# Performance work log

Hardware: AMD Instinct MI355X
Metric: run time of the kernel (lower is better)

## Reference

```python
import jax, jax.numpy as jnp
import numpy as np

B, N, E, D, H = 8, 50000, 200000, 64, 8

def setup_inputs() -> dict:
    key = jax.random.key(0)
    ks = jax.random.split(key, 6)
    X = jax.random.normal(ks[0], (B, N, D), dtype=jnp.float32)
    Ri_idx = jax.random.randint(ks[1], (B, E), 0, N, dtype=jnp.int64)
    Ro_idx = jax.random.randint(ks[2], (B, E), 0, N, dtype=jnp.int64)
    # MLP params: Linear(2D -> H), tanh, Linear(H -> 1), sigmoid
    W1 = jax.random.normal(ks[3], (2 * D, H), dtype=jnp.float32) * (1.0 / np.sqrt(2 * D))
    b1 = jnp.zeros((H,), dtype=jnp.float32)
    W2 = jax.random.normal(ks[4], (H, 1), dtype=jnp.float32) * (1.0 / np.sqrt(H))
    b2 = jnp.zeros((1,), dtype=jnp.float32)
    return {"X": X, "Ri_idx": Ri_idx, "Ro_idx": Ro_idx, "W1": W1, "b1": b1, "W2": W2, "b2": b2}

def reference(X, Ri_idx, Ro_idx, W1, b1, W2, b2):
    # spmm with one-hot incidence rows == gather of node features per edge
    bi = jnp.take_along_axis(X, Ri_idx[:, :, None], axis=1)  # [B,E,D]
    bo = jnp.take_along_axis(X, Ro_idx[:, :, None], axis=1)  # [B,E,D]
    Bfeat = jnp.concatenate([bo, bi], axis=-1)               # [B,E,2D]
    h = jnp.tanh(jnp.einsum('bed,dh->beh', Bfeat, W1) + b1)  # [B,E,H]
    out = jax.nn.sigmoid(jnp.einsum('beh,ho->beo', h, W2) + b2)  # [B,E,1]
    return out.squeeze(-1)  # [B,E]
```

## Files before the change

### kernel.cpp

```cpp
#include <hip/hip_runtime.h>
#include <hip/hip_bf16.h>

#define TILE 256

__device__ __forceinline__ float fast_tanh(float x) {
    float ax = fabsf(x);
    float t = __expf(-2.f * ax);
    float r = (1.f - t) * __builtin_amdgcn_rcpf(1.f + t);
    return copysignf(r, x);
}

__device__ __forceinline__ float fast_sigmoid(float s) {
    return __builtin_amdgcn_rcpf(1.f + __expf(-s));
}

__global__ __launch_bounds__(256, 2) void phase1_kernel(
    const float* __restrict__ X, const float* __restrict__ W1,
    const float* __restrict__ b1, float* __restrict__ P, int BN) {
    __shared__ float4 tile[TILE * 16];
    int t = threadIdx.x;
    int base = blockIdx.x * TILE;

#pragma unroll
    for (int k = 0; k < 16; ++k) {
        int s = t + (k << 8);
        int node = s >> 4;
        int f4 = s & 15;
        int gnode = base + node;
        gnode = (gnode < BN) ? gnode : (BN - 1);
        float4 v = *(const float4*)(X + ((size_t)gnode << 6) + (f4 << 2));
        tile[(node << 4) | (f4 ^ (node & 15))] = v;
    }
    __syncthreads();

    float acc[16];
#pragma unroll
    for (int j = 0; j < 8; ++j) acc[j] = b1[j];
#pragma unroll
    for (int j = 8; j < 16; ++j) acc[j] = 0.f;

    const float4* row = tile + (t << 4);
    int sw = t & 15;
#pragma unroll
    for (int dc4 = 0; dc4 < 16; ++dc4) {
        float4 xv = row[dc4 ^ sw];
#pragma unroll
        for (int dd = 0; dd < 4; ++dd) {
            int d = (dc4 << 2) + dd;
            float xs = (dd == 0) ? xv.x : (dd == 1) ? xv.y : (dd == 2) ? xv.z : xv.w;
            const float* wo = W1 + d * 8;
            const float* wi = W1 + (64 + d) * 8;
#pragma unroll
            for (int j = 0; j < 8; ++j) {
                acc[j]     += xs * wo[j];
                acc[8 + j] += xs * wi[j];
            }
        }
    }

    int gnode = base + t;
    if (gnode < BN) {
        float4* dst = (float4*)(P + ((size_t)gnode << 4));
        dst[0] = make_float4(acc[0],  acc[1],  acc[2],  acc[3]);
        dst[1] = make_float4(acc[4],  acc[5],  acc[6],  acc[7]);
        dst[2] = make_float4(acc[8],  acc[9],  acc[10], acc[11]);
        dst[3] = make_float4(acc[12], acc[13], acc[14], acc[15]);
    }
}

__global__ __launch_bounds__(256) void phase2_kernel(
    const int* __restrict__ Ri, const int* __restrict__ Ro,
    const float* __restrict__ P, const float* __restrict__ W2,
    const float* __restrict__ b2, float* __restrict__ out,
    int E, int N) {
    int b = blockIdx.x & 7;
    int e0 = (((blockIdx.x >> 3) << 8) + threadIdx.x) * 2;
    if (e0 >= E) return;
    size_t idx0 = (size_t)b * E + e0;
    int2 ro2 = *(const int2*)(Ro + idx0);
    int2 ri2 = *(const int2*)(Ri + idx0);

    float4 w2a = *(const float4*)W2;
    float4 w2b = *(const float4*)(W2 + 4);
    float bias2 = b2[0];
    const float4* Pv = (const float4*)P;
    int nb = b * N;

    float r[2];
#pragma unroll
    for (int k = 0; k < 2; ++k) {
        int ro = (k == 0) ? ro2.x : ro2.y;
        int ri = (k == 0) ? ri2.x : ri2.y;
        int robase = (nb + ro) << 2;
        int ribase = (nb + ri) << 2;
        float4 a0 = Pv[robase],     a1 = Pv[robase + 1];
        float4 c0 = Pv[ribase + 2], c1 = Pv[ribase + 3];
        float s = bias2;
        s += fast_tanh(a0.x + c0.x) * w2a.x;
        s += fast_tanh(a0.y + c0.y) * w2a.y;
        s += fast_tanh(a0.z + c0.z) * w2a.z;
        s += fast_tanh(a0.w + c0.w) * w2a.w;
        s += fast_tanh(a1.x + c1.x) * w2b.x;
        s += fast_tanh(a1.y + c1.y) * w2b.y;
        s += fast_tanh(a1.z + c1.z) * w2b.z;
        s += fast_tanh(a1.w + c1.w) * w2b.w;
        r[k] = fast_sigmoid(s);
    }
    *(float2*)(out + idx0) = make_float2(r[0], r[1]);
}

__global__ __launch_bounds__(256) void direct_kernel(
    const float* __restrict__ X, const int* __restrict__ Ri, const int* __restrict__ Ro,
    const float* __restrict__ W1, const float* __restrict__ b1,
    const float* __restrict__ W2, const float* __restrict__ b2,
    float* __restrict__ out, int E, int N) {
    int b = blockIdx.x & 7;
    int e = ((blockIdx.x >> 3) << 8) + threadIdx.x;
    if (e >= E) return;
    size_t idx = (size_t)b * E + e;
    int ro = Ro[idx], ri = Ri[idx];
    const float* xo = X + (size_t)(b * N + ro) * 64;
    const float* xi = X + (size_t)(b * N + ri) * 64;
    float acc[8];
#pragma unroll
    for (int j = 0; j < 8; ++j) acc[j] = b1[j];
#pragma unroll
    for (int dc = 0; dc < 64; dc += 4) {
        float4 ov = *(const float4*)(xo + dc);
        float4 iv = *(const float4*)(xi + dc);
#pragma unroll
        for (int dd = 0; dd < 4; ++dd) {
            float os = (dd == 0) ? ov.x : (dd == 1) ? ov.y : (dd == 2) ? ov.z : ov.w;
            float is = (dd == 0) ? iv.x : (dd == 1) ? iv.y : (dd == 2) ? iv.z : iv.w;
            const float* wo = W1 + (dc + dd) * 8;
            const float* wi = W1 + (64 + dc + dd) * 8;
#pragma unroll
            for (int j = 0; j < 8; ++j)
                acc[j] += os * wo[j] + is * wi[j];
        }
    }
    float4 w2a = *(const float4*)W2;
    float4 w2b = *(const float4*)(W2 + 4);
    float w2v[8] = {w2a.x, w2a.y, w2a.z, w2a.w, w2b.x, w2b.y, w2b.z, w2b.w};
    float s = b2[0];
#pragma unroll
    for (int j = 0; j < 8; ++j) s += fast_tanh(acc[j]) * w2v[j];
    out[idx] = fast_sigmoid(s);
}

extern "C" void kernel_launch(void* const* d_in, const int* in_sizes, int n_in,
                              void* d_out, int out_size, void* d_ws, size_t ws_size,
                              hipStream_t stream) {
    const float* X  = (const float*)d_in[0];
    const int*   Ri = (const int*)d_in[1];
    const int*   Ro = (const int*)d_in[2];
    const float* W1 = (const float*)d_in[3];
    const float* b1 = (const float*)d_in[4];
    const float* W2 = (const float*)d_in[5];
    const float* b2 = (const float*)d_in[6];
    float* out = (float*)d_out;

    const int B = 8;
    const int N = in_sizes[0] / (B * 64);
    const int E = in_sizes[1] / B;
    const int BN = B * N;

    size_t needP = (size_t)BN * 16 * sizeof(float);

    if (ws_size >= needP) {
        float* P = (float*)d_ws;
        int g1 = (BN + TILE - 1) / TILE;
        phase1_kernel<<<g1, 256, 0, stream>>>(X, W1, b1, P, BN);
        int bpb2 = (E + 511) / 512;
        phase2_kernel<<<8 * bpb2, 256, 0, stream>>>(Ri, Ro, P, W2, b2, out, E, N);
    } else {
        int bpb = (E + 255) / 256;
        direct_kernel<<<8 * bpb, 256, 0, stream>>>(X, Ri, Ro, W1, b1, W2, b2, out, E, N);
    }
}
```

Baseline: 201.7 us.

## Halve phase1 LDS tile with two-chunk staging and widen phase2 to four edges per thread

Phase1 now stages each node's 64 features in two 32-wide chunks, halving shared memory per block so more blocks can be resident, and reads X with nontemporal loads. Phase2 processes four edges per thread, issuing all eight gathers from P before any compute so more loads are in flight, and uses nontemporal loads for indices and a nontemporal store for the output. The costs are an extra barrier in phase1 and more registers per thread in phase2. Phase2's vector index loads rely on E being a multiple of 4.

New measurement: 189.9 us. -5.8%, faster.

```diff
diff --git a/kernel.cpp b/kernel.cpp
--- a/kernel.cpp
+++ b/kernel.cpp
@@ -2,6 +2,9 @@
 #include <hip/hip_bf16.h>
 
 #define TILE 256
+
+typedef float f32x4 __attribute__((ext_vector_type(4)));
+typedef int   i32x4 __attribute__((ext_vector_type(4)));
 
 __device__ __forceinline__ float fast_tanh(float x) {
     float ax = fabsf(x);
@@ -14,24 +17,12 @@
     return __builtin_amdgcn_rcpf(1.f + __expf(-s));
 }
 
-__global__ __launch_bounds__(256, 2) void phase1_kernel(
+__global__ __launch_bounds__(256) void phase1_kernel(
     const float* __restrict__ X, const float* __restrict__ W1,
     const float* __restrict__ b1, float* __restrict__ P, int BN) {
-    __shared__ float4 tile[TILE * 16];
+    __shared__ f32x4 lds[TILE * 8];
     int t = threadIdx.x;
     int base = blockIdx.x * TILE;
-
-#pragma unroll
-    for (int k = 0; k < 16; ++k) {
-        int s = t + (k << 8);
-        int node = s >> 4;
-        int f4 = s & 15;
-        int gnode = base + node;
-        gnode = (gnode < BN) ? gnode : (BN - 1);
-        float4 v = *(const float4*)(X + ((size_t)gnode << 6) + (f4 << 2));
-        tile[(node << 4) | (f4 ^ (node & 15))] = v;
-    }
-    __syncthreads();
 
     float acc[16];
 #pragma unroll
@@ -39,32 +30,50 @@
 #pragma unroll
     for (int j = 8; j < 16; ++j) acc[j] = 0.f;
 
-    const float4* row = tile + (t << 4);
-    int sw = t & 15;
+    const f32x4* Xv = (const f32x4*)X;
+    int sw = t & 7;
+
 #pragma unroll
-    for (int dc4 = 0; dc4 < 16; ++dc4) {
-        float4 xv = row[dc4 ^ sw];
+    for (int c = 0; c < 2; ++c) {
 #pragma unroll
-        for (int dd = 0; dd < 4; ++dd) {
-            int d = (dc4 << 2) + dd;
-            float xs = (dd == 0) ? xv.x : (dd == 1) ? xv.y : (dd == 2) ? xv.z : xv.w;
-            const float* wo = W1 + d * 8;
-            const float* wi = W1 + (64 + d) * 8;
+        for (int k = 0; k < 8; ++k) {
+            int s = t + (k << 8);
+            int node = s >> 3, f4l = s & 7;
+            int gn = base + node;
+            gn = (gn < BN) ? gn : (BN - 1);
+            f32x4 v = __builtin_nontemporal_load(
+                Xv + ((size_t)gn << 4) + (c << 3) + f4l);
+            lds[(node << 3) | (f4l ^ (node & 7))] = v;
+        }
+        __syncthreads();
+
+        const f32x4* row = lds + (t << 3);
 #pragma unroll
-            for (int j = 0; j < 8; ++j) {
-                acc[j]     += xs * wo[j];
-                acc[8 + j] += xs * wi[j];
+        for (int j8 = 0; j8 < 8; ++j8) {
+            f32x4 xv = row[j8 ^ sw];
+#pragma unroll
+            for (int dd = 0; dd < 4; ++dd) {
+                int d = (c << 5) + (j8 << 2) + dd;
+                float xs = xv[dd];
+                const float* wo = W1 + d * 8;
+                const float* wi = W1 + (64 + d) * 8;
+#pragma unroll
+                for (int j = 0; j < 8; ++j) {
+                    acc[j]     += xs * wo[j];
+                    acc[8 + j] += xs * wi[j];
+                }
             }
         }
+        if (c == 0) __syncthreads();
     }
 
     int gnode = base + t;
     if (gnode < BN) {
-        float4* dst = (float4*)(P + ((size_t)gnode << 4));
-        dst[0] = make_float4(acc[0],  acc[1],  acc[2],  acc[3]);
-        dst[1] = make_float4(acc[4],  acc[5],  acc[6],  acc[7]);
-        dst[2] = make_float4(acc[8],  acc[9],  acc[10], acc[11]);
-        dst[3] = make_float4(acc[12], acc[13], acc[14], acc[15]);
+        f32x4* dst = (f32x4*)(P + ((size_t)gnode << 4));
+        dst[0] = f32x4{acc[0],  acc[1],  acc[2],  acc[3]};
+        dst[1] = f32x4{acc[4],  acc[5],  acc[6],  acc[7]};
+        dst[2] = f32x4{acc[8],  acc[9],  acc[10], acc[11]};
+        dst[3] = f32x4{acc[12], acc[13], acc[14], acc[15]};
     }
 }
 
@@ -74,39 +83,38 @@
     const float* __restrict__ b2, float* __restrict__ out,
     int E, int N) {
     int b = blockIdx.x & 7;
-    int e0 = (((blockIdx.x >> 3) << 8) + threadIdx.x) * 2;
+    int e0 = (((blockIdx.x >> 3) << 8) + threadIdx.x) << 2;
     if (e0 >= E) return;
     size_t idx0 = (size_t)b * E + e0;
-    int2 ro2 = *(const int2*)(Ro + idx0);
-    int2 ri2 = *(const int2*)(Ri + idx0);
+    i32x4 ro4 = __builtin_nontemporal_load((const i32x4*)(Ro + idx0));
+    i32x4 ri4 = __builtin_nontemporal_load((const i32x4*)(Ri + idx0));
 
-    float4 w2a = *(const float4*)W2;
-    float4 w2b = *(const float4*)(W2 + 4);
+    const f32x4* Pv = (const f32x4*)P;
+    int nb = b * N;
+    f32x4 a0[4], a1[4], c0[4], c1[4];
+#pragma unroll
+    for (int k = 0; k < 4; ++k) {
+        int rb = (nb + ro4[k]) << 2;
+        int ib = (nb + ri4[k]) << 2;
+        a0[k] = Pv[rb];     a1[k] = Pv[rb + 1];
+        c0[k] = Pv[ib + 2]; c1[k] = Pv[ib + 3];
+    }
+
+    f32x4 w2a = *(const f32x4*)W2;
+    f32x4 w2b = *(const f32x4*)(W2 + 4);
     float bias2 = b2[0];
-    const float4* Pv = (const float4*)P;
-    int nb = b * N;
-
-    float r[2];
+    f32x4 res;
 #pragma unroll
-    for (int k = 0; k < 2; ++k) {
-        int ro = (k == 0) ? ro2.x : ro2.y;
-        int ri = (k == 0) ? ri2.x : ri2.y;
-        int robase = (nb + ro) << 2;
-        int ribase = (nb + ri) << 2;
-        float4 a0 = Pv[robase],     a1 = Pv[robase + 1];
-        float4 c0 = Pv[ribase + 2], c1 = Pv[ribase + 3];
+    for (int k = 0; k < 4; ++k) {
         float s = bias2;
-        s += fast_tanh(a0.x + c0.x) * w2a.x;
-        s += fast_tanh(a0.y + c0.y) * w2a.y;
-        s += fast_tanh(a0.z + c0.z) * w2a.z;
-        s += fast_tanh(a0.w + c0.w) * w2a.w;
-        s += fast_tanh(a1.x + c1.x) * w2b.x;
-        s += fast_tanh(a1.y + c1.y) * w2b.y;
-        s += fast_tanh(a1.z + c1.z) * w2b.z;
-        s += fast_tanh(a1.w + c1.w) * w2b.w;
-        r[k] = fast_sigmoid(s);
+#pragma unroll
+        for (int j = 0; j < 4; ++j) {
+            s += fast_tanh(a0[k][j] + c0[k][j]) * w2a[j];
+            s += fast_tanh(a1[k][j] + c1[k][j]) * w2b[j];
+        }
+        res[k] = fast_sigmoid(s);
     }
-    *(float2*)(out + idx0) = make_float2(r[0], r[1]);
+    __builtin_nontemporal_store(res, (f32x4*)(out + idx0));
 }
 
 __global__ __launch_bounds__(256) void direct_kernel(
@@ -171,7 +179,7 @@
         float* P = (float*)d_ws;
         int g1 = (BN + TILE - 1) / TILE;
         phase1_kernel<<<g1, 256, 0, stream>>>(X, W1, b1, P, BN);
-        int bpb2 = (E + 511) / 512;
+        int bpb2 = (E + 1023) / 1024;
         phase2_kernel<<<8 * bpb2, 256, 0, stream>>>(Ri, Ro, P, W2, b2, out, E, N);
     } else {
         int bpb = (E + 255) / 256;
```
